# Kernel optimization log

Hardware: AMD Instinct MI355X
Metric: run time of the kernel (lower is better)

## Reference

```python
import math
import jax, jax.numpy as jnp
import numpy as np

N_HEADS = 16  # matches init_kwargs n_heads

def setup_inputs() -> dict:
    key = jax.random.key(0)
    ks = jax.random.split(key, 6)
    B, T, D = 1, 2048, 1024
    x = jax.random.normal(ks[0], (B, T, D), dtype=jnp.float32)
    # binary causal mask, broadcast over batch: [B, T, T]
    mask = jnp.broadcast_to(jnp.tril(jnp.ones((T, T), dtype=jnp.float32)), (B, T, T))
    shift = jax.random.uniform(ks[1], (B, T, T), dtype=jnp.float32)
    W = jax.random.normal(ks[2], (D, 3 * D), dtype=jnp.float32) * (1.0 / math.sqrt(D))
    b = jnp.zeros((3 * D,), dtype=jnp.float32)
    Wo = jax.random.normal(ks[3], (D, D), dtype=jnp.float32) * (1.0 / math.sqrt(D))
    bo = jnp.zeros((D,), dtype=jnp.float32)
    return {"x": x, "mask": mask, "shift": shift, "W": W, "b": b, "Wo": Wo, "bo": bo}

def reference(x, mask, shift, W, b, Wo, bo):
    B, T, D = x.shape
    H = N_HEADS
    dh = D // H
    qkv = x @ W + b  # [B,T,3D]
    # torch: chunk(H) -> stack -> chunk(3): head h uses block [h*3*dh : (h+1)*3*dh],
    # split as (q, k, v) of size dh each => reshape last dim to (H, 3, dh)
    qkv = qkv.reshape(B, T, H, 3, dh)
    q = jnp.moveaxis(qkv[..., 0, :], 2, 0)  # [H,B,T,dh]
    k = jnp.moveaxis(qkv[..., 1, :], 2, 0)
    v = jnp.moveaxis(qkv[..., 2, :], 2, 0)
    logits = jnp.einsum('hbqd,hbkd->hbqk', q, k) / math.sqrt(dh)  # [H,B,T,T]
    logits = logits * mask - 1e6 * (1.0 - mask)  # mask [B,T,T] broadcasts over H
    # per-head ALiBi-like scale: exp(-log(2) * h / 2)
    scale = jnp.exp(-math.log(2.0) * jnp.arange(H, dtype=jnp.float32) / 2.0)
    logits = logits - scale.reshape(H, 1, 1, 1) * shift
    att = jax.nn.softmax(logits, axis=-1)
    o = jnp.einsum('hbqk,hbkd->hbqd', att, v)  # [H,B,T,dh]
    o = jnp.moveaxis(o, 0, 2).reshape(B, T, D)  # concat heads on last dim
    o = o @ Wo + bo
    k_out = jnp.moveaxis(k, 0, 2).reshape(B, T, D)
    v_out = jnp.moveaxis(v, 0, 2).reshape(B, T, D)
    return (o, k_out, v_out)
```

## Files before the change

### kernel.cpp

```cpp
#include <hip/hip_runtime.h>
#include <hip/hip_bf16.h>

typedef __attribute__((ext_vector_type(8))) short bfrag8;
typedef __attribute__((ext_vector_type(4))) short short4v;
typedef __attribute__((ext_vector_type(4))) float f32x4;
typedef __attribute__((ext_vector_type(8))) unsigned short ushort8;
typedef __attribute__((ext_vector_type(4))) unsigned short ushort4v;
typedef __attribute__((ext_vector_type(2))) unsigned int uint2v;

__device__ __forceinline__ float bf2f(unsigned short u) {
  unsigned int v = ((unsigned int)u) << 16;
  return __builtin_bit_cast(float, v);
}
__device__ __forceinline__ unsigned short f2bf(float f) {
  unsigned int u = __builtin_bit_cast(unsigned int, f);
  u += 0x7fffu + ((u >> 16) & 1u);
  return (unsigned short)(u >> 16);
}
__device__ __forceinline__ unsigned int cvtpk_bf16(float a, float b) {
  unsigned int r;
  asm("v_cvt_pk_bf16_f32 %0, %1, %2" : "=v"(r) : "v"(a), "v"(b));
  return r;
}

#define GLDS(gp, lp) __builtin_amdgcn_global_load_lds( \
    (__attribute__((address_space(1))) void*)(gp), \
    (__attribute__((address_space(3))) void*)(lp), 16, 0, 0)

#define WAIT_LGKM0() __builtin_amdgcn_s_waitcnt(0xc07f)

__device__ __forceinline__ bool inputs_are_f32(const unsigned int* mw) {
  return mw[0] == 0x3F800000u;
}

__global__ __launch_bounds__(256) void prep_kernel(
    const void* __restrict__ x, const void* __restrict__ b,
    const void* __restrict__ bo, const void* __restrict__ W,
    const void* __restrict__ Wo,
    unsigned short* __restrict__ xc, unsigned short* __restrict__ bc,
    unsigned short* __restrict__ boc, unsigned short* __restrict__ Wt,
    unsigned short* __restrict__ Wot,
    const unsigned int* __restrict__ mw) {
  const bool isf32 = inputs_are_f32(mw);
  const int bid = blockIdx.x, tid = threadIdx.x;
  __shared__ unsigned short tile[64][72];

  if (bid < 2052) {
    const void* src; unsigned short* dst; int base, n4;
    if (bid < 2048)      { src = x;  dst = xc;  base = bid;        n4 = 2048 * 1024 / 4; }
    else if (bid < 2051) { src = b;  dst = bc;  base = bid - 2048; n4 = 3072 / 4; }
    else                 { src = bo; dst = boc; base = 0;          n4 = 1024 / 4; }
    int i = base * 256 + tid;
    if (i >= n4) return;
    ushort4v o;
    if (isf32) {
      const float* s = (const float*)src;
      o[0] = f2bf(s[i * 4 + 0]); o[1] = f2bf(s[i * 4 + 1]);
      o[2] = f2bf(s[i * 4 + 2]); o[3] = f2bf(s[i * 4 + 3]);
    } else {
      o = *(const ushort4v*)((const unsigned short*)src + (size_t)i * 4);
    }
    *(ushort4v*)(dst + (size_t)i * 4) = o;
    return;
  }

  const void* src; unsigned short* dst; int R, C, bx, by;
  if (bid < 2820) { src = W;  dst = Wt;  R = 1024; C = 3072;
                    int e = bid - 2052; bx = e % 48; by = e / 48; }
  else            { src = Wo; dst = Wot; R = 1024; C = 1024;
                    int e = bid - 2820; bx = e % 16; by = e / 16; }
  const int r0 = by << 6, c0 = bx << 6;
  #pragma unroll
  for (int i = 0; i < 16; ++i) {
    int e = i * 256 + tid;
    int r = e >> 6, c = e & 63;
    size_t idx = (size_t)(r0 + r) * C + c0 + c;
    tile[r][c] = isf32 ? f2bf(((const float*)src)[idx])
                       : ((const unsigned short*)src)[idx];
  }
  __syncthreads();
  #pragma unroll
  for (int i = 0; i < 16; ++i) {
    int e = i * 256 + tid;
    int c = e >> 6, r = e & 63;
    dst[(size_t)(c0 + c) * R + r0 + r] = tile[r][c];
  }
}

template <int BM, int BN, int EPI>
__global__ __launch_bounds__(256) void gemm_bt(
    const unsigned short* __restrict__ A,
    const unsigned short* __restrict__ Bt,
    const unsigned short* __restrict__ bias,
    unsigned short* __restrict__ Cbf,
    float* __restrict__ kout,
    float* __restrict__ vout,
    float* __restrict__ Cf,
    int M, int N, int K) {
  constexpr int MI = BM / 32;
  constexpr int NT = BN / 32;
  __shared__ __align__(16) unsigned short As[BM * 32];
  __shared__ __align__(16) unsigned short Bs[BN * 32];
  const int tid = threadIdx.x;
  const int wave = tid >> 6, lane = tid & 63;
  const int q8 = lane >> 4, l15 = lane & 15;
  const int m0 = blockIdx.y * BM, n0 = blockIdx.x * BN;
  const int wm = (wave >> 1) * (BM / 2), wn = (wave & 1) * (BN / 2);

  f32x4 acc[MI][NT];
  #pragma unroll
  for (int i = 0; i < MI; ++i)
    #pragma unroll
    for (int t = 0; t < NT; ++t) acc[i][t] = (f32x4){0.f, 0.f, 0.f, 0.f};

  const int cidb = wave * 64 + lane;
  for (int k0 = 0; k0 < K; k0 += 32) {
    __syncthreads();
    #pragma unroll
    for (int j = 0; j < BM / 64; ++j) {
      int cid = j * 256 + cidb;
      int row = cid >> 2, co = (cid & 3) << 3;
      GLDS(A + (size_t)(m0 + row) * K + k0 + co, As + (size_t)(j * 256 + wave * 64) * 8);
    }
    #pragma unroll
    for (int j = 0; j < BN / 64; ++j) {
      int cid = j * 256 + cidb;
      int row = cid >> 2, co = (cid & 3) << 3;
      GLDS(Bt + (size_t)(n0 + row) * K + k0 + co, Bs + (size_t)(j * 256 + wave * 64) * 8);
    }
    __builtin_amdgcn_s_waitcnt(0);
    __syncthreads();
    bfrag8 af[MI], bfr[NT];
    #pragma unroll
    for (int i = 0; i < MI; ++i)
      af[i] = *(const bfrag8*)(As + (wm + i * 16 + l15) * 32 + q8 * 8);
    #pragma unroll
    for (int t = 0; t < NT; ++t)
      bfr[t] = *(const bfrag8*)(Bs + (wn + t * 16 + l15) * 32 + q8 * 8);
    #pragma unroll
    for (int i = 0; i < MI; ++i)
      #pragma unroll
      for (int t = 0; t < NT; ++t)
        acc[i][t] = __builtin_amdgcn_mfma_f32_16x16x32_bf16(af[i], bfr[t], acc[i][t], 0, 0, 0);
  }

  #pragma unroll
  for (int t = 0; t < NT; ++t) {
    const int col = n0 + wn + t * 16 + l15;
    const float bv = bf2f(bias[col]);
    #pragma unroll
    for (int i = 0; i < MI; ++i) {
      #pragma unroll
      for (int r = 0; r < 4; ++r) {
        const int row = m0 + wm + i * 16 + q8 * 4 + r;
        const float fv = acc[i][t][r] + bv;
        if (EPI) {
          Cbf[(size_t)row * N + col] = f2bf(fv);
          int h = col / 192, rr = col - h * 192;
          if (rr >= 128)      vout[(size_t)row * 1024 + h * 64 + (rr - 128)] = fv;
          else if (rr >= 64)  kout[(size_t)row * 1024 + h * 64 + (rr - 64)] = fv;
        } else {
          Cf[(size_t)row * N + col] = fv;
        }
      }
    }
  }
}

__global__ __launch_bounds__(256) void attn_kernel(
    const unsigned short* __restrict__ qkv,
    const void* __restrict__ shift,
    unsigned short* __restrict__ Pon,
    float* __restrict__ Mst,
    float* __restrict__ Lst,
    const unsigned int* __restrict__ mw) {
  const bool isf32 = inputs_are_f32(mw);
  __shared__ __align__(16) unsigned short Qs[64 * 64];
  __shared__ __align__(16) unsigned short Ks[64 * 64];
  __shared__ __align__(16) unsigned short VTs[64 * 64];
  __shared__ __align__(16) short Ps[4 * 16 * 64];

  const int tid = threadIdx.x;
  const int wave = tid >> 6, lane = tid & 63;
  const int q8 = lane >> 4, l15 = lane & 15;
  int rem = blockIdx.x;
  int qb = 31;
  for (;;) { int seg = ((qb + 6) / 6) << 4; if (rem < seg) break; rem -= seg; --qb; }
  const int p = rem >> 4, h = rem & 15;
  const int q0 = qb << 6;
  const int count = qb + 1;
  const int kbeg = p * 6;
  const int kend = (kbeg + 6 < count) ? (kbeg + 6) : count;
  const float LOG2E = 1.4426950408889634f;
  const float c1 = 0.125f * LOG2E;
  const float scale2 = __builtin_amdgcn_exp2f(-0.5f * (float)h) * LOG2E;
  const float NEG = -1e30f;

  #pragma unroll
  for (int j = 0; j < 2; ++j) {
    int cid = j * 256 + wave * 64 + lane;
    int row = cid >> 3, ci = cid & 7;
    ushort8 qv = *(const ushort8*)(qkv + (size_t)(q0 + row) * 3072 + h * 192 + ci * 8);
    *(ushort8*)(Qs + row * 64 + ((ci ^ (row & 7)) << 3)) = qv;
  }

  const int cidA = wave * 64 + lane;
  const int rowA = cidA >> 3, ciA = cidA & 7;
  const int cidB = 256 + cidA;
  const int rowB = cidB >> 3, ciB = cidB & 7;

  float mrow = NEG, lrow = 0.f;
  f32x4 oacc[4];
  #pragma unroll
  for (int t = 0; t < 4; ++t) oacc[t] = (f32x4){0.f, 0.f, 0.f, 0.f};
  const int qg = q0 + wave * 16 + l15;

  ushort8 kpfA, kpfB, vpf0, vpf1;
  float shf[4][4];

  {
    const int k0 = kbeg << 6;
    kpfA = *(const ushort8*)(qkv + (size_t)(k0 + rowA) * 3072 + h * 192 + 64 + ciA * 8);
    kpfB = *(const ushort8*)(qkv + (size_t)(k0 + rowB) * 3072 + h * 192 + 64 + ciB * 8);
    const unsigned short* vsrc = qkv + (size_t)(k0 + lane) * 3072 + h * 192 + 128 + wave * 16;
    vpf0 = *(const ushort8*)(vsrc);
    vpf1 = *(const ushort8*)(vsrc + 8);
    if (isf32) {
      const float* sp = (const float*)shift + (size_t)qg * 2048 + k0 + q8 * 4;
      #pragma unroll
      for (int mt = 0; mt < 4; ++mt) {
        f32x4 t4 = *(const f32x4*)(sp + mt * 16);
        shf[mt][0] = scale2 * t4[0]; shf[mt][1] = scale2 * t4[1];
        shf[mt][2] = scale2 * t4[2]; shf[mt][3] = scale2 * t4[3];
      }
    } else {
      const unsigned short* sp = (const unsigned short*)shift + (size_t)qg * 2048 + k0 + q8 * 4;
      #pragma unroll
      for (int mt = 0; mt < 4; ++mt) {
        ushort4v t4 = *(const ushort4v*)(sp + mt * 16);
        shf[mt][0] = scale2 * bf2f(t4[0]); shf[mt][1] = scale2 * bf2f(t4[1]);
        shf[mt][2] = scale2 * bf2f(t4[2]); shf[mt][3] = scale2 * bf2f(t4[3]);
      }
    }
  }

  for (int kt = kbeg; kt < kend; ++kt) {
    const int k0 = kt << 6;
    WAIT_LGKM0();
    __builtin_amdgcn_s_barrier();
    *(ushort8*)(Ks + rowA * 64 + ((ciA ^ (rowA & 7)) << 3)) = kpfA;
    *(ushort8*)(Ks + rowB * 64 + ((ciB ^ (rowB & 7)) << 3)) = kpfB;
    #pragma unroll
    for (int j = 0; j < 8; ++j) {
      int d = wave * 16 + j;
      VTs[d * 64 + (((lane >> 3) ^ (d & 7)) << 3) + (lane & 7)] = vpf0[j];
      int d2 = d + 8;
      VTs[d2 * 64 + (((lane >> 3) ^ (d2 & 7)) << 3) + (lane & 7)] = vpf1[j];
    }
    WAIT_LGKM0();
    __builtin_amdgcn_s_barrier();

    if (kt + 1 < kend) {
      const int k0n = k0 + 64;
      kpfA = *(const ushort8*)(qkv + (size_t)(k0n + rowA) * 3072 + h * 192 + 64 + ciA * 8);
      kpfB = *(const ushort8*)(qkv + (size_t)(k0n + rowB) * 3072 + h * 192 + 64 + ciB * 8);
      const unsigned short* vsrc = qkv + (size_t)(k0n + lane) * 3072 + h * 192 + 128 + wave * 16;
      vpf0 = *(const ushort8*)(vsrc);
      vpf1 = *(const ushort8*)(vsrc + 8);
    }

    f32x4 st[4];
    #pragma unroll
    for (int mt = 0; mt < 4; ++mt) st[mt] = (f32x4){0.f, 0.f, 0.f, 0.f};
    __builtin_amdgcn_s_setprio(1);
    #pragma unroll
    for (int kk = 0; kk < 2; ++kk) {
      int kc = kk * 4 + q8;
      int qrow = wave * 16 + l15;
      bfrag8 bq = *(const bfrag8*)(Qs + qrow * 64 + ((kc ^ (qrow & 7)) << 3));
      #pragma unroll
      for (int mt = 0; mt < 4; ++mt) {
        int krow = mt * 16 + l15;
        bfrag8 ak = *(const bfrag8*)(Ks + krow * 64 + ((kc ^ (krow & 7)) << 3));
        st[mt] = __builtin_amdgcn_mfma_f32_16x16x32_bf16(ak, bq, st[mt], 0, 0, 0);
      }
    }
    __builtin_amdgcn_s_setprio(0);

    const bool diag = (kt == qb);
    float sv[4][4];
    float tmax = NEG;
    #pragma unroll
    for (int mt = 0; mt < 4; ++mt)
      #pragma unroll
      for (int r = 0; r < 4; ++r) {
        float s = st[mt][r] * c1 - shf[mt][r];
        if (diag) {
          int kg = k0 + mt * 16 + q8 * 4 + r;
          if (kg > qg) s = NEG;
        }
        sv[mt][r] = s;
        tmax = fmaxf(tmax, s);
      }

    if (kt + 1 < kend) {
      const int k0n = k0 + 64;
      if (isf32) {
        const float* sp = (const float*)shift + (size_t)qg * 2048 + k0n + q8 * 4;
        #pragma unroll
        for (int mt = 0; mt < 4; ++mt) {
          f32x4 t4 = *(const f32x4*)(sp + mt * 16);
          shf[mt][0] = scale2 * t4[0]; shf[mt][1] = scale2 * t4[1];
          shf[mt][2] = scale2 * t4[2]; shf[mt][3] = scale2 * t4[3];
        }
      } else {
        const unsigned short* sp = (const unsigned short*)shift + (size_t)qg * 2048 + k0n + q8 * 4;
        #pragma unroll
        for (int mt = 0; mt < 4; ++mt) {
          ushort4v t4 = *(const ushort4v*)(sp + mt * 16);
          shf[mt][0] = scale2 * bf2f(t4[0]); shf[mt][1] = scale2 * bf2f(t4[1]);
          shf[mt][2] = scale2 * bf2f(t4[2]); shf[mt][3] = scale2 * bf2f(t4[3]);
        }
      }
    }

    tmax = fmaxf(tmax, __shfl_xor(tmax, 16, 64));
    tmax = fmaxf(tmax, __shfl_xor(tmax, 32, 64));
    const int skip = __all(tmax - mrow <= 8.0f);
    const float mnew = skip ? mrow : fmaxf(mrow, tmax);
    float psum = 0.f;
    #pragma unroll
    for (int mt = 0; mt < 4; ++mt)
      #pragma unroll
      for (int r = 0; r < 4; ++r) {
        float pv = __builtin_amdgcn_exp2f(sv[mt][r] - mnew);
        sv[mt][r] = pv;
        psum += pv;
      }
    psum += __shfl_xor(psum, 16, 64);
    psum += __shfl_xor(psum, 32, 64);

    short* pw = Ps + wave * 1024;
    #pragma unroll
    for (int mt = 0; mt < 4; ++mt) {
      unsigned int w0 = cvtpk_bf16(sv[mt][0], sv[mt][1]);
      unsigned int w1 = cvtpk_bf16(sv[mt][2], sv[mt][3]);
      uint2v u2; u2[0] = w0; u2[1] = w1;
      short4v pk = __builtin_bit_cast(short4v, u2);
      int kb = mt * 16 + q8 * 4;
      int chunk = (kb >> 3) ^ (l15 & 7);
      *(short4v*)(pw + l15 * 64 + (chunk << 3) + (kb & 7)) = pk;
    }

    if (skip) {
      lrow += psum;
    } else {
      const float alpha = __builtin_amdgcn_exp2f(mrow - mnew);
      lrow = lrow * alpha + psum;
      mrow = mnew;
      float oal[4];
      #pragma unroll
      for (int r = 0; r < 4; ++r)
        oal[r] = __shfl(alpha, (lane & 48) | (q8 * 4 + r), 64);
      #pragma unroll
      for (int t = 0; t < 4; ++t)
        #pragma unroll
        for (int r = 0; r < 4; ++r) oacc[t][r] *= oal[r];
    }

    WAIT_LGKM0();

    __builtin_amdgcn_s_setprio(1);
    #pragma unroll
    for (int kk = 0; kk < 2; ++kk) {
      int kc = kk * 4 + q8;
      bfrag8 ap = *(const bfrag8*)(pw + l15 * 64 + ((kc ^ (l15 & 7)) << 3));
      #pragma unroll
      for (int t = 0; t < 4; ++t) {
        int drow = t * 16 + l15;
        bfrag8 bv = *(const bfrag8*)(VTs + drow * 64 + ((kc ^ (drow & 7)) << 3));
        oacc[t] = __builtin_amdgcn_mfma_f32_16x16x32_bf16(ap, bv, oacc[t], 0, 0, 0);
      }
    }
    __builtin_amdgcn_s_setprio(0);
  }

  float linv[4];
  #pragma unroll
  for (int r = 0; r < 4; ++r) {
    float lr = __shfl(lrow, (lane & 48) | (q8 * 4 + r), 64);
    linv[r] = lr > 0.f ? 1.f / lr : 0.f;
  }
  const size_t slot = (size_t)(h * 32 + qb) * 6 + p;
  const size_t pbase = slot * 4096;
  #pragma unroll
  for (int t = 0; t < 4; ++t)
    #pragma unroll
    for (int r = 0; r < 4; ++r) {
      int rowl = wave * 16 + q8 * 4 + r;
      int coll = t * 16 + l15;
      Pon[pbase + rowl * 64 + coll] = f2bf(oacc[t][r] * linv[r]);
    }
  if (q8 == 0) {
    const size_t sbase = slot * 64 + wave * 16 + l15;
    Mst[sbase] = mrow;
    Lst[sbase] = lrow;
  }
}

__global__ __launch_bounds__(256) void attn_merge(
    const unsigned short* __restrict__ Pon,
    const float* __restrict__ Mst, const float* __restrict__ Lst,
    unsigned short* __restrict__ oheads) {
  const int bid = blockIdx.x;
  const int h = bid >> 5, qb = bid & 31;
  const int np = (qb + 6) / 6;
  const int t = threadIdx.x;
  const int q = t >> 2, dp = (t & 3) << 4;
  const size_t slot0 = (size_t)(h * 32 + qb) * 6;
  float mv[6], lv[6];
  float m = -1e30f;
  #pragma unroll
  for (int p = 0; p < 6; ++p) {
    mv[p] = (p < np) ? Mst[(slot0 + p) * 64 + q] : -1e30f;
    lv[p] = (p < np) ? Lst[(slot0 + p) * 64 + q] : 0.f;
    m = fmaxf(m, mv[p]);
  }
  float w[6], wsum = 0.f;
  #pragma unroll
  for (int p = 0; p < 6; ++p) {
    w[p] = __builtin_amdgcn_exp2f(mv[p] - m) * lv[p];
    wsum += w[p];
  }
  const float inv = 1.f / wsum;
  float acc0[8], acc1[8];
  #pragma unroll
  for (int j = 0; j < 8; ++j) { acc0[j] = 0.f; acc1[j] = 0.f; }
  #pragma unroll
  for (int p = 0; p < 6; ++p) {
    if (p < np) {
      const unsigned short* pp = Pon + (slot0 + p) * 4096 + q * 64 + dp;
      ushort8 a0 = *(const ushort8*)pp;
      ushort8 a1 = *(const ushort8*)(pp + 8);
      #pragma unroll
      for (int j = 0; j < 8; ++j) {
        acc0[j] += w[p] * bf2f(a0[j]);
        acc1[j] += w[p] * bf2f(a1[j]);
      }
    }
  }
  unsigned short* dst = oheads + (size_t)(qb * 64 + q) * 1024 + h * 64 + dp;
  ushort8 o0, o1;
  #pragma unroll
  for (int j = 0; j < 8; ++j) {
    o0[j] = f2bf(acc0[j] * inv);
    o1[j] = f2bf(acc1[j] * inv);
  }
  *(ushort8*)dst = o0;
  *(ushort8*)(dst + 8) = o1;
}

extern "C" void kernel_launch(void* const* d_in, const int* in_sizes, int n_in,
                              void* d_out, int out_size, void* d_ws, size_t ws_size,
                              hipStream_t stream) {
  const void* x     = d_in[0];
  const unsigned int* maskw = (const unsigned int*)d_in[1];
  const void* shift = d_in[2];
  const void* W     = d_in[3];
  const void* b     = d_in[4];
  const void* Wo    = d_in[5];
  const void* bo    = d_in[6];

  float* out   = (float*)d_out;
  float* o_out = out;
  float* k_out = out + (size_t)2048 * 1024;
  float* v_out = out + (size_t)2 * 2048 * 1024;

  unsigned short* ws     = (unsigned short*)d_ws;
  unsigned short* qkv    = ws;
  unsigned short* Wot    = qkv + (size_t)2048 * 3072;
  unsigned short* oheads = Wot + (size_t)1024 * 1024;
  unsigned short* bc     = oheads + (size_t)2048 * 1024;
  unsigned short* boc    = bc + 3072;
  unsigned short* xc     = boc + 1024;
  unsigned short* Wt     = xc + (size_t)2048 * 1024;
  unsigned short* Pon    = xc;
  float*          Mst    = (float*)(Pon + (size_t)16 * 32 * 6 * 4096);
  float*          Lst    = Mst + 196608;

  prep_kernel<<<3076, 256, 0, stream>>>(x, b, bo, W, Wo,
                                        xc, bc, boc, Wt, Wot, maskw);

  gemm_bt<64, 128, 1><<<dim3(24, 32), 256, 0, stream>>>(
      xc, Wt, bc, qkv, k_out, v_out, nullptr, 2048, 3072, 1024);

  attn_kernel<<<1632, 256, 0, stream>>>(qkv, shift, Pon, Mst, Lst, maskw);

  attn_merge<<<512, 256, 0, stream>>>(Pon, Mst, Lst, oheads);

  gemm_bt<64, 64, 0><<<dim3(16, 32), 256, 0, stream>>>(
      oheads, Wot, boc, nullptr, nullptr, nullptr, o_out, 2048, 1024, 1024);
}
```

Before: 197.5 us.

## Keep softmax P in registers via permuted key rows; widen GEMM K-tile with swizzle

The attention kernel permutes which key rows each MFMA tile computes so that the S accumulator layout matches the A-operand layout of the PV MFMA. The bf16-packed probabilities can then feed the second MFMA straight from registers, which removes the LDS round trip, the Ps buffer and an LDS wait. Shift loads and the causal mask index are remapped to follow the permutation. Separately, the GEMM K-tile grows from 32 to 64 with an XOR-swizzled LDS layout to halve the barriers per K and avoid bank conflicts, at the cost of more LDS per block.

```diff
diff --git a/kernel.cpp b/kernel.cpp
--- a/kernel.cpp
+++ b/kernel.cpp
@@ -2,11 +2,10 @@
 #include <hip/hip_bf16.h>
 
 typedef __attribute__((ext_vector_type(8))) short bfrag8;
-typedef __attribute__((ext_vector_type(4))) short short4v;
 typedef __attribute__((ext_vector_type(4))) float f32x4;
 typedef __attribute__((ext_vector_type(8))) unsigned short ushort8;
 typedef __attribute__((ext_vector_type(4))) unsigned short ushort4v;
-typedef __attribute__((ext_vector_type(2))) unsigned int uint2v;
+typedef __attribute__((ext_vector_type(4))) unsigned int uint4v;
 
 __device__ __forceinline__ float bf2f(unsigned short u) {
   unsigned int v = ((unsigned int)u) << 16;
@@ -87,7 +86,7 @@
   }
 }
 
-template <int BM, int BN, int EPI>
+template <int BM, int BN, int BK, int EPI>
 __global__ __launch_bounds__(256) void gemm_bt(
     const unsigned short* __restrict__ A,
     const unsigned short* __restrict__ Bt,
@@ -99,13 +98,15 @@
     int M, int N, int K) {
   constexpr int MI = BM / 32;
   constexpr int NT = BN / 32;
-  __shared__ __align__(16) unsigned short As[BM * 32];
-  __shared__ __align__(16) unsigned short Bs[BN * 32];
+  constexpr int CW = BK / 8;
+  __shared__ __align__(16) unsigned short As[BM * BK];
+  __shared__ __align__(16) unsigned short Bs[BN * BK];
   const int tid = threadIdx.x;
   const int wave = tid >> 6, lane = tid & 63;
   const int q8 = lane >> 4, l15 = lane & 15;
   const int m0 = blockIdx.y * BM, n0 = blockIdx.x * BN;
   const int wm = (wave >> 1) * (BM / 2), wn = (wave & 1) * (BN / 2);
+  const int swz = l15 & 7;
 
   f32x4 acc[MI][NT];
   #pragma unroll
@@ -114,34 +115,40 @@
     for (int t = 0; t < NT; ++t) acc[i][t] = (f32x4){0.f, 0.f, 0.f, 0.f};
 
   const int cidb = wave * 64 + lane;
-  for (int k0 = 0; k0 < K; k0 += 32) {
+  for (int k0 = 0; k0 < K; k0 += BK) {
     __syncthreads();
     #pragma unroll
-    for (int j = 0; j < BM / 64; ++j) {
+    for (int j = 0; j < (BM * BK) / 2048; ++j) {
       int cid = j * 256 + cidb;
-      int row = cid >> 2, co = (cid & 3) << 3;
-      GLDS(A + (size_t)(m0 + row) * K + k0 + co, As + (size_t)(j * 256 + wave * 64) * 8);
-    }
-    #pragma unroll
-    for (int j = 0; j < BN / 64; ++j) {
+      int row = cid / CW, p = cid % CW;
+      GLDS(A + (size_t)(m0 + row) * K + k0 + ((p ^ (row & 7)) << 3),
+           As + (size_t)(j * 256 + wave * 64) * 8);
+    }
+    #pragma unroll
+    for (int j = 0; j < (BN * BK) / 2048; ++j) {
       int cid = j * 256 + cidb;
-      int row = cid >> 2, co = (cid & 3) << 3;
-      GLDS(Bt + (size_t)(n0 + row) * K + k0 + co, Bs + (size_t)(j * 256 + wave * 64) * 8);
+      int row = cid / CW, p = cid % CW;
+      GLDS(Bt + (size_t)(n0 + row) * K + k0 + ((p ^ (row & 7)) << 3),
+           Bs + (size_t)(j * 256 + wave * 64) * 8);
     }
     __builtin_amdgcn_s_waitcnt(0);
     __syncthreads();
-    bfrag8 af[MI], bfr[NT];
-    #pragma unroll
-    for (int i = 0; i < MI; ++i)
-      af[i] = *(const bfrag8*)(As + (wm + i * 16 + l15) * 32 + q8 * 8);
-    #pragma unroll
-    for (int t = 0; t < NT; ++t)
-      bfr[t] = *(const bfrag8*)(Bs + (wn + t * 16 + l15) * 32 + q8 * 8);
-    #pragma unroll
-    for (int i = 0; i < MI; ++i)
+    #pragma unroll
+    for (int kk = 0; kk < BK / 32; ++kk) {
+      const int kc = kk * 4 + q8;
+      bfrag8 af[MI], bfr[NT];
+      #pragma unroll
+      for (int i = 0; i < MI; ++i)
+        af[i] = *(const bfrag8*)(As + (size_t)(wm + i * 16 + l15) * BK + ((kc ^ swz) << 3));
       #pragma unroll
       for (int t = 0; t < NT; ++t)
-        acc[i][t] = __builtin_amdgcn_mfma_f32_16x16x32_bf16(af[i], bfr[t], acc[i][t], 0, 0, 0);
+        bfr[t] = *(const bfrag8*)(Bs + (size_t)(wn + t * 16 + l15) * BK + ((kc ^ swz) << 3));
+      #pragma unroll
+      for (int i = 0; i < MI; ++i)
+        #pragma unroll
+        for (int t = 0; t < NT; ++t)
+          acc[i][t] = __builtin_amdgcn_mfma_f32_16x16x32_bf16(af[i], bfr[t], acc[i][t], 0, 0, 0);
+    }
   }
 
   #pragma unroll
@@ -178,7 +185,6 @@
   __shared__ __align__(16) unsigned short Qs[64 * 64];
   __shared__ __align__(16) unsigned short Ks[64 * 64];
   __shared__ __align__(16) unsigned short VTs[64 * 64];
-  __shared__ __align__(16) short Ps[4 * 16 * 64];
 
   const int tid = threadIdx.x;
   const int wave = tid >> 6, lane = tid & 63;
@@ -195,6 +201,8 @@
   const float c1 = 0.125f * LOG2E;
   const float scale2 = __builtin_amdgcn_exp2f(-0.5f * (float)h) * LOG2E;
   const float NEG = -1e30f;
+  const int moff0 = 0, moff1 = 32, moff2 = 4, moff3 = 36;
+  const int base_l = ((l15 >> 2) << 3) + (l15 & 3);
 
   #pragma unroll
   for (int j = 0; j < 2; ++j) {
@@ -226,20 +234,26 @@
     vpf0 = *(const ushort8*)(vsrc);
     vpf1 = *(const ushort8*)(vsrc + 8);
     if (isf32) {
-      const float* sp = (const float*)shift + (size_t)qg * 2048 + k0 + q8 * 4;
-      #pragma unroll
-      for (int mt = 0; mt < 4; ++mt) {
-        f32x4 t4 = *(const f32x4*)(sp + mt * 16);
-        shf[mt][0] = scale2 * t4[0]; shf[mt][1] = scale2 * t4[1];
-        shf[mt][2] = scale2 * t4[2]; shf[mt][3] = scale2 * t4[3];
+      const float* sp = (const float*)shift + (size_t)qg * 2048 + k0 + q8 * 8;
+      f32x4 t0 = *(const f32x4*)(sp + moff0);
+      f32x4 t1 = *(const f32x4*)(sp + moff1);
+      f32x4 t2 = *(const f32x4*)(sp + moff2);
+      f32x4 t3 = *(const f32x4*)(sp + moff3);
+      #pragma unroll
+      for (int r = 0; r < 4; ++r) {
+        shf[0][r] = scale2 * t0[r]; shf[1][r] = scale2 * t1[r];
+        shf[2][r] = scale2 * t2[r]; shf[3][r] = scale2 * t3[r];
       }
     } else {
-      const unsigned short* sp = (const unsigned short*)shift + (size_t)qg * 2048 + k0 + q8 * 4;
-      #pragma unroll
-      for (int mt = 0; mt < 4; ++mt) {
-        ushort4v t4 = *(const ushort4v*)(sp + mt * 16);
-        shf[mt][0] = scale2 * bf2f(t4[0]); shf[mt][1] = scale2 * bf2f(t4[1]);
-        shf[mt][2] = scale2 * bf2f(t4[2]); shf[mt][3] = scale2 * bf2f(t4[3]);
+      const unsigned short* sp = (const unsigned short*)shift + (size_t)qg * 2048 + k0 + q8 * 8;
+      ushort4v t0 = *(const ushort4v*)(sp + moff0);
+      ushort4v t1 = *(const ushort4v*)(sp + moff1);
+      ushort4v t2 = *(const ushort4v*)(sp + moff2);
+      ushort4v t3 = *(const ushort4v*)(sp + moff3);
+      #pragma unroll
+      for (int r = 0; r < 4; ++r) {
+        shf[0][r] = scale2 * bf2f(t0[r]); shf[1][r] = scale2 * bf2f(t1[r]);
+        shf[2][r] = scale2 * bf2f(t2[r]); shf[3][r] = scale2 * bf2f(t3[r]);
       }
     }
   }
@@ -280,7 +294,8 @@
       bfrag8 bq = *(const bfrag8*)(Qs + qrow * 64 + ((kc ^ (qrow & 7)) << 3));
       #pragma unroll
       for (int mt = 0; mt < 4; ++mt) {
-        int krow = mt * 16 + l15;
+        const int mo = (mt == 0) ? moff0 : (mt == 1) ? moff1 : (mt == 2) ? moff2 : moff3;
+        int krow = base_l + mo;
         bfrag8 ak = *(const bfrag8*)(Ks + krow * 64 + ((kc ^ (krow & 7)) << 3));
         st[mt] = __builtin_amdgcn_mfma_f32_16x16x32_bf16(ak, bq, st[mt], 0, 0, 0);
       }
@@ -291,35 +306,43 @@
     float sv[4][4];
     float tmax = NEG;
     #pragma unroll
-    for (int mt = 0; mt < 4; ++mt)
+    for (int mt = 0; mt < 4; ++mt) {
+      const int mo = (mt == 0) ? moff0 : (mt == 1) ? moff1 : (mt == 2) ? moff2 : moff3;
       #pragma unroll
       for (int r = 0; r < 4; ++r) {
         float s = st[mt][r] * c1 - shf[mt][r];
         if (diag) {
-          int kg = k0 + mt * 16 + q8 * 4 + r;
+          int kg = k0 + (q8 << 3) + mo + r;
           if (kg > qg) s = NEG;
         }
         sv[mt][r] = s;
         tmax = fmaxf(tmax, s);
       }
+    }
 
     if (kt + 1 < kend) {
       const int k0n = k0 + 64;
       if (isf32) {
-        const float* sp = (const float*)shift + (size_t)qg * 2048 + k0n + q8 * 4;
+        const float* sp = (const float*)shift + (size_t)qg * 2048 + k0n + q8 * 8;
+        f32x4 t0 = *(const f32x4*)(sp + moff0);
+        f32x4 t1 = *(const f32x4*)(sp + moff1);
+        f32x4 t2 = *(const f32x4*)(sp + moff2);
+        f32x4 t3 = *(const f32x4*)(sp + moff3);
         #pragma unroll
-        for (int mt = 0; mt < 4; ++mt) {
-          f32x4 t4 = *(const f32x4*)(sp + mt * 16);
-          shf[mt][0] = scale2 * t4[0]; shf[mt][1] = scale2 * t4[1];
-          shf[mt][2] = scale2 * t4[2]; shf[mt][3] = scale2 * t4[3];
+        for (int r = 0; r < 4; ++r) {
+          shf[0][r] = scale2 * t0[r]; shf[1][r] = scale2 * t1[r];
+          shf[2][r] = scale2 * t2[r]; shf[3][r] = scale2 * t3[r];
         }
       } else {
-        const unsigned short* sp = (const unsigned short*)shift + (size_t)qg * 2048 + k0n + q8 * 4;
+        const unsigned short* sp = (const unsigned short*)shift + (size_t)qg * 2048 + k0n + q8 * 8;
+        ushort4v t0 = *(const ushort4v*)(sp + moff0);
+        ushort4v t1 = *(const ushort4v*)(sp + moff1);
+        ushort4v t2 = *(const ushort4v*)(sp + moff2);
+        ushort4v t3 = *(const ushort4v*)(sp + moff3);
         #pragma unroll
-        for (int mt = 0; mt < 4; ++mt) {
-          ushort4v t4 = *(const ushort4v*)(sp + mt * 16);
-          shf[mt][0] = scale2 * bf2f(t4[0]); shf[mt][1] = scale2 * bf2f(t4[1]);
-          shf[mt][2] = scale2 * bf2f(t4[2]); shf[mt][3] = scale2 * bf2f(t4[3]);
+        for (int r = 0; r < 4; ++r) {
+          shf[0][r] = scale2 * bf2f(t0[r]); shf[1][r] = scale2 * bf2f(t1[r]);
+          shf[2][r] = scale2 * bf2f(t2[r]); shf[3][r] = scale2 * bf2f(t3[r]);
         }
       }
     }
@@ -340,17 +363,18 @@
     psum += __shfl_xor(psum, 16, 64);
     psum += __shfl_xor(psum, 32, 64);
 
-    short* pw = Ps + wave * 1024;
-    #pragma unroll
-    for (int mt = 0; mt < 4; ++mt) {
-      unsigned int w0 = cvtpk_bf16(sv[mt][0], sv[mt][1]);
-      unsigned int w1 = cvtpk_bf16(sv[mt][2], sv[mt][3]);
-      uint2v u2; u2[0] = w0; u2[1] = w1;
-      short4v pk = __builtin_bit_cast(short4v, u2);
-      int kb = mt * 16 + q8 * 4;
-      int chunk = (kb >> 3) ^ (l15 & 7);
-      *(short4v*)(pw + l15 * 64 + (chunk << 3) + (kb & 7)) = pk;
-    }
+    const unsigned int w00 = cvtpk_bf16(sv[0][0], sv[0][1]);
+    const unsigned int w01 = cvtpk_bf16(sv[0][2], sv[0][3]);
+    const unsigned int w10 = cvtpk_bf16(sv[1][0], sv[1][1]);
+    const unsigned int w11 = cvtpk_bf16(sv[1][2], sv[1][3]);
+    const unsigned int w20 = cvtpk_bf16(sv[2][0], sv[2][1]);
+    const unsigned int w21 = cvtpk_bf16(sv[2][2], sv[2][3]);
+    const unsigned int w30 = cvtpk_bf16(sv[3][0], sv[3][1]);
+    const unsigned int w31 = cvtpk_bf16(sv[3][2], sv[3][3]);
+    uint4v u0; u0[0] = w00; u0[1] = w01; u0[2] = w20; u0[3] = w21;
+    uint4v u1; u1[0] = w10; u1[1] = w11; u1[2] = w30; u1[3] = w31;
+    const bfrag8 ap0 = __builtin_bit_cast(bfrag8, u0);
+    const bfrag8 ap1 = __builtin_bit_cast(bfrag8, u1);
 
     if (skip) {
       lrow += psum;
@@ -368,13 +392,11 @@
         for (int r = 0; r < 4; ++r) oacc[t][r] *= oal[r];
     }
 
-    WAIT_LGKM0();
-
     __builtin_amdgcn_s_setprio(1);
     #pragma unroll
     for (int kk = 0; kk < 2; ++kk) {
       int kc = kk * 4 + q8;
-      bfrag8 ap = *(const bfrag8*)(pw + l15 * 64 + ((kc ^ (l15 & 7)) << 3));
+      const bfrag8 ap = kk ? ap1 : ap0;
       #pragma unroll
       for (int t = 0; t < 4; ++t) {
         int drow = t * 16 + l15;
@@ -491,13 +513,13 @@
   prep_kernel<<<3076, 256, 0, stream>>>(x, b, bo, W, Wo,
                                         xc, bc, boc, Wt, Wot, maskw);
 
-  gemm_bt<64, 128, 1><<<dim3(24, 32), 256, 0, stream>>>(
+  gemm_bt<64, 128, 64, 1><<<dim3(24, 32), 256, 0, stream>>>(
       xc, Wt, bc, qkv, k_out, v_out, nullptr, 2048, 3072, 1024);
 
   attn_kernel<<<1632, 256, 0, stream>>>(qkv, shift, Pon, Mst, Lst, maskw);
 
   attn_merge<<<512, 256, 0, stream>>>(Pon, Mst, Lst, oheads);
 
-  gemm_bt<64, 64, 0><<<dim3(16, 32), 256, 0, stream>>>(
+  gemm_bt<64, 64, 64, 0><<<dim3(16, 32), 256, 0, stream>>>(
       oheads, Wot, boc, nullptr, nullptr, nullptr, o_out, 2048, 1024, 1024);
 }
```

Result: faster. 187.7 us (-5.0%).
